# Performance work log

Hardware: AMD Instinct MI355X
Metric: run time of the kernel (lower is better)

## Reference

```python
import jax, jax.numpy as jnp
import numpy as np

B, C, D = 512, 1000, 512
K = 10


def setup_inputs() -> dict:
    key = jax.random.key(0)
    k1, k2, k3, k4, k5 = jax.random.split(key, 5)
    x = jax.random.normal(k1, (B, D), dtype=jnp.float32)
    protos = jax.random.normal(k2, (C, D), dtype=jnp.float32)
    # ex2/ex1 chosen so N*ex2^2 - ex1^2 > 0 (valid sqrt)
    ex2 = jax.random.uniform(k3, (C, D), dtype=jnp.float32) + 1.0
    ex1 = jax.random.uniform(k4, (C, D), dtype=jnp.float32) * 0.1
    cls_num = jax.random.randint(k5, (C,), 1, 100, dtype=jnp.int32)
    proto_label = jnp.arange(C, dtype=jnp.int32)
    return {"x": x, "protos": protos, "ex2": ex2, "ex1": ex1,
            "cls_num": cls_num, "proto_label": proto_label, "k_nearest": K}


def reference(x, protos, ex2, ex1, cls_num, proto_label, k_nearest):
    # rd: per-class, per-feature variance proxy  [C, D]
    N = cls_num[:, None].astype(ex2.dtype)
    rd = jnp.sqrt(N * ex2 ** 2 - ex1 ** 2)
    # softmax over feature dim of (rowmax - rd)
    rd = jax.nn.softmax(jnp.max(rd, axis=1, keepdims=True) - rd, axis=1)
    # weighted squared distances: [B, C, D] -> reduce D -> [B, C]
    diff = x[:, None, :] - protos[None, :, :]
    x_dists = diff ** 2 * rd[None, :, :]
    simi_mat = x_dists.sum(axis=2)  # [B, C]
    # k smallest distances (torch.topk largest=False)
    neg_vals, topk_index = jax.lax.top_k(-simi_mat, k_nearest)
    topk_vals = -neg_vals  # [B, K]
    topk_conf = topk_vals.sum(axis=1, keepdims=True) / topk_vals  # [B, K]
    # pick prototype with max confidence, map through label table
    temp = jnp.argmax(topk_conf, axis=1)  # [B]
    ans_index = jnp.take_along_axis(topk_index, temp[:, None], axis=1)[:, 0]
    predict = proto_label[ans_index]  # [B]
    return predict, topk_conf
```

## Files before the change

### kernel.cpp

```cpp
#include <hip/hip_runtime.h>
#include <math.h>
#include <float.h>

#define B_SZ 512
#define C_SZ 1000
#define D_SZ 512
#define K_TOP 10
#define K2 1024
#define NSPLIT 4
#define KSPLIT 256
#define BC (B_SZ * C_SZ)

#define T3_OFF 0
#define PART_OFF 1024

#define BM 64
#define BN 64
#define BK 32
#define LDA 40
#define LDB 264

using f16x8 = __attribute__((ext_vector_type(8))) _Float16;
using f32x4 = __attribute__((ext_vector_type(4))) float;

#if __has_builtin(__builtin_amdgcn_exp2f)
#define FAST_EXP2(x) __builtin_amdgcn_exp2f(x)
#else
#define FAST_EXP2(x) exp2f(x)
#endif
#if __has_builtin(__builtin_amdgcn_sqrtf)
#define FAST_SQRT(x) __builtin_amdgcn_sqrtf(x)
#else
#define FAST_SQRT(x) sqrtf(x)
#endif
#define LOG2E 1.44269504088896340736f

__device__ __forceinline__ void split2(float v, _Float16& h, _Float16& l) {
    h = (_Float16)v;
    l = (_Float16)(v - (float)h);
}

__global__ __launch_bounds__(256, 2) void gemm_fused(const float* __restrict__ x,
                                                     const float* __restrict__ protos,
                                                     const float* __restrict__ ex2,
                                                     const float* __restrict__ ex1,
                                                     const int* __restrict__ cls_num,
                                                     float* __restrict__ ws) {
    __shared__ __align__(16) _Float16 Ah[BM][LDA];
    __shared__ __align__(16) _Float16 Al[BM][LDA];
    __shared__ __align__(16) _Float16 BSh[BN][LDB];
    __shared__ __align__(16) _Float16 BSl[BN][LDB];

    float* t3   = ws + T3_OFF;
    float* part = ws + PART_OFF;

    const int tid  = threadIdx.x;
    const int lane = tid & 63;
    const int w    = tid >> 6;
    const int c0 = blockIdx.x * BN;
    const int b0 = blockIdx.y * BM;
    const int kz = blockIdx.z;
    const bool isRd = (kz < 2);
    const int ownBase = isRd ? kz * 32 : (kz - 2) * 32;
    const int dutyLo = blockIdx.y * 8;

    for (int i = 0; i < 16; i++) {
        const int lc = w * 16 + i;
        const int c  = c0 + lc;
        if (c < C_SZ) {
            const size_t rb = (size_t)c * D_SZ + lane * 8;
            float e2v[8], e1v[8], pv[8];
            *(float4*)&e2v[0] = *(const float4*)(ex2 + rb);
            *(float4*)&e2v[4] = *(const float4*)(ex2 + rb + 4);
            *(float4*)&e1v[0] = *(const float4*)(ex1 + rb);
            *(float4*)&e1v[4] = *(const float4*)(ex1 + rb + 4);
            *(float4*)&pv[0]  = *(const float4*)(protos + rb);
            *(float4*)&pv[4]  = *(const float4*)(protos + rb + 4);
            const float N = (float)cls_num[c];

            float v[8], mn = FLT_MAX;
            #pragma unroll
            for (int k = 0; k < 8; k++) {
                v[k] = FAST_SQRT(N * e2v[k] * e2v[k] - e1v[k] * e1v[k]);
                mn = fminf(mn, v[k]);
            }
            #pragma unroll
            for (int off = 1; off < 64; off <<= 1) mn = fminf(mn, __shfl_xor(mn, off));

            float ev[8], s = 0.f;
            #pragma unroll
            for (int k = 0; k < 8; k++) {
                ev[k] = FAST_EXP2((mn - v[k]) * LOG2E);
                s += ev[k];
            }

            const bool duty = (kz == 0) && (lc >= dutyLo) && (lc < dutyLo + 8);
            if (duty) {
                float te = 0.f;
                #pragma unroll
                for (int k = 0; k < 8; k++) te = fmaf(ev[k] * pv[k], pv[k], te);
                #pragma unroll
                for (int off = 1; off < 64; off <<= 1) {
                    s  += __shfl_xor(s, off);
                    te += __shfl_xor(te, off);
                }
                const float inv = 1.0f / s;
                if (lane == 0) t3[c] = te * inv;
                const int rel = lane - ownBase;
                if (rel >= 0 && rel < 32) {
                    f16x8 hh, ll;
                    #pragma unroll
                    for (int k = 0; k < 8; k++) {
                        const float rdv = ev[k] * inv;
                        const float val = isRd ? rdv : (-2.0f * rdv * pv[k]);
                        _Float16 h, l;
                        split2(val, h, l);
                        hh[k] = h; ll[k] = l;
                    }
                    *(f16x8*)&BSh[lc][rel * 8] = hh;
                    *(f16x8*)&BSl[lc][rel * 8] = ll;
                }
            } else {
                #pragma unroll
                for (int off = 1; off < 64; off <<= 1) s += __shfl_xor(s, off);
                const float inv = 1.0f / s;
                const int rel = lane - ownBase;
                if (rel >= 0 && rel < 32) {
                    f16x8 hh, ll;
                    #pragma unroll
                    for (int k = 0; k < 8; k++) {
                        const float rdv = ev[k] * inv;
                        const float val = isRd ? rdv : (-2.0f * rdv * pv[k]);
                        _Float16 h, l;
                        split2(val, h, l);
                        hh[k] = h; ll[k] = l;
                    }
                    *(f16x8*)&BSh[lc][rel * 8] = hh;
                    *(f16x8*)&BSl[lc][rel * 8] = ll;
                }
            }
        } else {
            if (lane < 32) {
                f16x8 z;
                #pragma unroll
                for (int k = 0; k < 8; k++) z[k] = (_Float16)0.f;
                *(f16x8*)&BSh[lc][lane * 8] = z;
                *(f16x8*)&BSl[lc][lane * 8] = z;
            }
        }
    }
    __syncthreads();

    const int khalf0 = isRd ? kz * KSPLIT : kz * KSPLIT - D_SZ;
    const int srow = tid >> 2;
    const int sseg = (tid & 3) * 8;
    const int mw = (w >> 1) * 32;
    const int nw = (w & 1) * 32;
    const int lr = lane & 15;
    const int kg = lane >> 4;

    f32x4 acc[2][2];
    #pragma unroll
    for (int i = 0; i < 2; i++)
        #pragma unroll
        for (int j = 0; j < 2; j++)
            #pragma unroll
            for (int r = 0; r < 4; r++) acc[i][j][r] = 0.f;

    for (int ch = 0; ch < KSPLIT / BK; ch++) {
        const int kx = khalf0 + ch * BK + sseg;

        float4 a0 = *(const float4*)(x + (size_t)(b0 + srow) * D_SZ + kx);
        float4 a1 = *(const float4*)(x + (size_t)(b0 + srow) * D_SZ + kx + 4);
        if (isRd) {
            a0.x *= a0.x; a0.y *= a0.y; a0.z *= a0.z; a0.w *= a0.w;
            a1.x *= a1.x; a1.y *= a1.y; a1.z *= a1.z; a1.w *= a1.w;
        }
        const float av[8] = {a0.x, a0.y, a0.z, a0.w, a1.x, a1.y, a1.z, a1.w};
        f16x8 ah, al;
        #pragma unroll
        for (int j = 0; j < 8; j++) {
            _Float16 hh, ll;
            split2(av[j], hh, ll);
            ah[j] = hh; al[j] = ll;
        }

        __syncthreads();
        *(f16x8*)&Ah[srow][sseg] = ah;
        *(f16x8*)&Al[srow][sseg] = al;
        __syncthreads();

        f16x8 fah[2], fal[2], fbh[2], fbl[2];
        #pragma unroll
        for (int i = 0; i < 2; i++) {
            fah[i] = *(const f16x8*)&Ah[mw + i * 16 + lr][kg * 8];
            fal[i] = *(const f16x8*)&Al[mw + i * 16 + lr][kg * 8];
            fbh[i] = *(const f16x8*)&BSh[nw + i * 16 + lr][ch * BK + kg * 8];
            fbl[i] = *(const f16x8*)&BSl[nw + i * 16 + lr][ch * BK + kg * 8];
        }
        #pragma unroll
        for (int i = 0; i < 2; i++)
            #pragma unroll
            for (int j = 0; j < 2; j++) {
                acc[i][j] = __builtin_amdgcn_mfma_f32_16x16x32_f16(fal[i], fbl[j], acc[i][j], 0, 0, 0);
                acc[i][j] = __builtin_amdgcn_mfma_f32_16x16x32_f16(fah[i], fbl[j], acc[i][j], 0, 0, 0);
                acc[i][j] = __builtin_amdgcn_mfma_f32_16x16x32_f16(fal[i], fbh[j], acc[i][j], 0, 0, 0);
                acc[i][j] = __builtin_amdgcn_mfma_f32_16x16x32_f16(fah[i], fbh[j], acc[i][j], 0, 0, 0);
            }
    }

    float* o = part + (size_t)kz * BC;
    #pragma unroll
    for (int i = 0; i < 2; i++) {
        #pragma unroll
        for (int j = 0; j < 2; j++) {
            const int c = c0 + nw + j * 16 + lr;
            if (c < C_SZ) {
                #pragma unroll
                for (int r = 0; r < 4; r++) {
                    const int b = b0 + mw + i * 16 + kg * 4 + r;
                    o[(size_t)b * C_SZ + c] = acc[i][j][r];
                }
            }
        }
    }
}

__global__ __launch_bounds__(256) void topk_kernel(const float* __restrict__ ws,
                                                   const int* __restrict__ proto_label,
                                                   float* __restrict__ out) {
    const float* part = ws + PART_OFF;
    const float* t3   = ws + T3_OFF;
    const int wid = threadIdx.x >> 6;
    const int lane = threadIdx.x & 63;
    const int b = blockIdx.x * 4 + wid;

    float vals[16];
    #pragma unroll
    for (int j = 0; j < 16; j++) {
        const int c = lane + j * 64;
        if (c < C_SZ) {
            const size_t idx = (size_t)b * C_SZ + c;
            float s = t3[c];
            #pragma unroll
            for (int z = 0; z < NSPLIT; z++)
                s += part[(size_t)z * BC + idx];
            vals[j] = s;
        } else {
            vals[j] = FLT_MAX;
        }
    }

    float kv[K_TOP];
    int ki[K_TOP];
    for (int t = 0; t < K_TOP; t++) {
        float bv = FLT_MAX;
        int bi = 0x7fffffff;
        #pragma unroll
        for (int j = 0; j < 16; j++) {
            const int c = lane + j * 64;
            if (vals[j] < bv) { bv = vals[j]; bi = c; }
        }
        #pragma unroll
        for (int off = 1; off < 64; off <<= 1) {
            const float ov = __shfl_xor(bv, off);
            const int oi = __shfl_xor(bi, off);
            if (ov < bv || (ov == bv && oi < bi)) { bv = ov; bi = oi; }
        }
        kv[t] = bv;
        ki[t] = bi;
        if ((bi & 63) == lane) vals[bi >> 6] = FLT_MAX;
    }

    if (lane == 0) {
        float S = 0.f;
        #pragma unroll
        for (int t = 0; t < K_TOP; t++) S += kv[t];
        float conf[K_TOP];
        #pragma unroll
        for (int t = 0; t < K_TOP; t++) {
            conf[t] = S / kv[t];
            out[B_SZ + b * K_TOP + t] = conf[t];
        }
        int best = 0;
        for (int t = 1; t < K_TOP; t++)
            if (conf[t] > conf[best]) best = t;
        out[b] = (float)proto_label[ki[best]];
    }
}

extern "C" void kernel_launch(void* const* d_in, const int* in_sizes, int n_in,
                              void* d_out, int out_size, void* d_ws, size_t ws_size,
                              hipStream_t stream) {
    const float* x           = (const float*)d_in[0];
    const float* protos      = (const float*)d_in[1];
    const float* ex2         = (const float*)d_in[2];
    const float* ex1         = (const float*)d_in[3];
    const int*   cls_num     = (const int*)d_in[4];
    const int*   proto_label = (const int*)d_in[5];

    float* ws  = (float*)d_ws;
    float* out = (float*)d_out;

    dim3 g((C_SZ + BN - 1) / BN, B_SZ / BM, NSPLIT);
    gemm_fused<<<g, 256, 0, stream>>>(x, protos, ex2, ex1, cls_num, ws);

    topk_kernel<<<B_SZ / 4, 256, 0, stream>>>(ws, proto_label, out);
}
```

Measured before the change: 107.0 us.

## Fuse weight prep, GEMM and top-k into one kernel with flag-based grid sync

Merges the two launches into one persistent-style kernel. Only kz==0 blocks compute the softmax weights, each for 8 classes, and write them to global memory; the other blocks spin on per-tile flags before loading them. This removes the redundant per-block weight recomputation and the second kernel launch. The top-k step is done by kz==3 blocks after they spin on partial-completion flags. It relies on all 512 blocks being co-resident to avoid deadlock, adds spin-wait latency, and never resets the flags, so stale MAGIC values from a previous call could let later calls read unfinished data.

```diff
diff --git a/kernel.cpp b/kernel.cpp
--- a/kernel.cpp
+++ b/kernel.cpp
@@ -11,8 +11,13 @@
 #define KSPLIT 256
 #define BC (B_SZ * C_SZ)
 
-#define T3_OFF 0
-#define PART_OFF 1024
+#define WHI_OFFH 0
+#define WLO_OFFH (1024 * 1024)
+#define FLAGB_OFF 1048576
+#define FLAGP_OFF (FLAGB_OFF + 256)
+#define T3_OFF    (FLAGB_OFF + 1024)
+#define PART_OFF  (T3_OFF + 1024)
+#define MAGIC 0x5F3C0DE5u
 
 #define BM 64
 #define BN 64
@@ -40,65 +45,65 @@
     l = (_Float16)(v - (float)h);
 }
 
-__global__ __launch_bounds__(256, 2) void gemm_fused(const float* __restrict__ x,
-                                                     const float* __restrict__ protos,
-                                                     const float* __restrict__ ex2,
-                                                     const float* __restrict__ ex1,
-                                                     const int* __restrict__ cls_num,
-                                                     float* __restrict__ ws) {
+__global__ __launch_bounds__(256, 2) void fused_all(const float* __restrict__ x,
+                                                    const float* __restrict__ protos,
+                                                    const float* __restrict__ ex2,
+                                                    const float* __restrict__ ex1,
+                                                    const int* __restrict__ cls_num,
+                                                    const int* __restrict__ proto_label,
+                                                    float* __restrict__ ws,
+                                                    float* __restrict__ out) {
     __shared__ __align__(16) _Float16 Ah[BM][LDA];
     __shared__ __align__(16) _Float16 Al[BM][LDA];
     __shared__ __align__(16) _Float16 BSh[BN][LDB];
     __shared__ __align__(16) _Float16 BSl[BN][LDB];
 
+    _Float16* Whi = (_Float16*)ws + WHI_OFFH;
+    _Float16* Wlo = (_Float16*)ws + WLO_OFFH;
+    unsigned int* flagB = (unsigned int*)(ws + FLAGB_OFF);
+    unsigned int* flagP = (unsigned int*)(ws + FLAGP_OFF);
     float* t3   = ws + T3_OFF;
     float* part = ws + PART_OFF;
 
     const int tid  = threadIdx.x;
     const int lane = tid & 63;
     const int w    = tid >> 6;
-    const int c0 = blockIdx.x * BN;
-    const int b0 = blockIdx.y * BM;
-    const int kz = blockIdx.z;
+    const int cx = blockIdx.x, by = blockIdx.y, kz = blockIdx.z;
+    const int c0 = cx * BN;
+    const int b0 = by * BM;
     const bool isRd = (kz < 2);
-    const int ownBase = isRd ? kz * 32 : (kz - 2) * 32;
-    const int dutyLo = blockIdx.y * 8;
-
-    for (int i = 0; i < 16; i++) {
-        const int lc = w * 16 + i;
-        const int c  = c0 + lc;
-        if (c < C_SZ) {
-            const size_t rb = (size_t)c * D_SZ + lane * 8;
-            float e2v[8], e1v[8], pv[8];
-            *(float4*)&e2v[0] = *(const float4*)(ex2 + rb);
-            *(float4*)&e2v[4] = *(const float4*)(ex2 + rb + 4);
-            *(float4*)&e1v[0] = *(const float4*)(ex1 + rb);
-            *(float4*)&e1v[4] = *(const float4*)(ex1 + rb + 4);
-            *(float4*)&pv[0]  = *(const float4*)(protos + rb);
-            *(float4*)&pv[4]  = *(const float4*)(protos + rb + 4);
-            const float N = (float)cls_num[c];
-
-            float v[8], mn = FLT_MAX;
-            #pragma unroll
-            for (int k = 0; k < 8; k++) {
-                v[k] = FAST_SQRT(N * e2v[k] * e2v[k] - e1v[k] * e1v[k]);
-                mn = fminf(mn, v[k]);
-            }
-            #pragma unroll
-            for (int off = 1; off < 64; off <<= 1) mn = fminf(mn, __shfl_xor(mn, off));
-
-            float ev[8], s = 0.f;
-            #pragma unroll
-            for (int k = 0; k < 8; k++) {
-                ev[k] = FAST_EXP2((mn - v[k]) * LOG2E);
-                s += ev[k];
-            }
-
-            const bool duty = (kz == 0) && (lc >= dutyLo) && (lc < dutyLo + 8);
-            if (duty) {
-                float te = 0.f;
-                #pragma unroll
-                for (int k = 0; k < 8; k++) te = fmaf(ev[k] * pv[k], pv[k], te);
+
+    if (kz == 0) {
+        #pragma unroll
+        for (int r = 0; r < 2; r++) {
+            const int c = c0 + by * 8 + w * 2 + r;
+            if (c < C_SZ) {
+                const size_t rb = (size_t)c * D_SZ + lane * 8;
+                float e2v[8], e1v[8], pv[8];
+                *(float4*)&e2v[0] = *(const float4*)(ex2 + rb);
+                *(float4*)&e2v[4] = *(const float4*)(ex2 + rb + 4);
+                *(float4*)&e1v[0] = *(const float4*)(ex1 + rb);
+                *(float4*)&e1v[4] = *(const float4*)(ex1 + rb + 4);
+                *(float4*)&pv[0]  = *(const float4*)(protos + rb);
+                *(float4*)&pv[4]  = *(const float4*)(protos + rb + 4);
+                const float N = (float)cls_num[c];
+
+                float v[8], mn = FLT_MAX;
+                #pragma unroll
+                for (int k = 0; k < 8; k++) {
+                    v[k] = FAST_SQRT(N * e2v[k] * e2v[k] - e1v[k] * e1v[k]);
+                    mn = fminf(mn, v[k]);
+                }
+                #pragma unroll
+                for (int off = 1; off < 64; off <<= 1) mn = fminf(mn, __shfl_xor(mn, off));
+
+                float ev[8], s = 0.f, te = 0.f;
+                #pragma unroll
+                for (int k = 0; k < 8; k++) {
+                    ev[k] = FAST_EXP2((mn - v[k]) * LOG2E);
+                    s += ev[k];
+                    te = fmaf(ev[k] * pv[k], pv[k], te);
+                }
                 #pragma unroll
                 for (int off = 1; off < 64; off <<= 1) {
                     s  += __shfl_xor(s, off);
@@ -106,53 +111,64 @@
                 }
                 const float inv = 1.0f / s;
                 if (lane == 0) t3[c] = te * inv;
-                const int rel = lane - ownBase;
-                if (rel >= 0 && rel < 32) {
-                    f16x8 hh, ll;
-                    #pragma unroll
-                    for (int k = 0; k < 8; k++) {
-                        const float rdv = ev[k] * inv;
-                        const float val = isRd ? rdv : (-2.0f * rdv * pv[k]);
-                        _Float16 h, l;
-                        split2(val, h, l);
-                        hh[k] = h; ll[k] = l;
-                    }
-                    *(f16x8*)&BSh[lc][rel * 8] = hh;
-                    *(f16x8*)&BSl[lc][rel * 8] = ll;
-                }
+
+                f16x8 h1, l1, h2, l2;
+                #pragma unroll
+                for (int k = 0; k < 8; k++) {
+                    const float rdv = ev[k] * inv;
+                    const float w2  = -2.0f * rdv * pv[k];
+                    _Float16 hh, ll;
+                    split2(rdv, hh, ll); h1[k] = hh; l1[k] = ll;
+                    split2(w2,  hh, ll); h2[k] = hh; l2[k] = ll;
+                }
+                _Float16* wh = Whi + (size_t)c * K2 + lane * 8;
+                _Float16* wl = Wlo + (size_t)c * K2 + lane * 8;
+                *(f16x8*)(wh)         = h1;
+                *(f16x8*)(wh + D_SZ)  = h2;
+                *(f16x8*)(wl)         = l1;
+                *(f16x8*)(wl + D_SZ)  = l2;
+            }
+        }
+        __syncthreads();
+        if (tid == 0) {
+            __threadfence();
+            __hip_atomic_store(&flagB[cx * 8 + by], MAGIC,
+                               __ATOMIC_RELEASE, __HIP_MEMORY_SCOPE_AGENT);
+        }
+    }
+
+    if (w == 0 && lane < 8) {
+        for (int it = 0; it < (1 << 22); ++it) {
+            if (__hip_atomic_load(&flagB[cx * 8 + lane], __ATOMIC_RELAXED,
+                                  __HIP_MEMORY_SCOPE_AGENT) == MAGIC) break;
+            __builtin_amdgcn_s_sleep(4);
+        }
+    }
+    __syncthreads();
+    __threadfence();
+
+    const int srow = tid >> 2;
+    const int cseg = (tid & 3) * 8;
+    {
+        const int c = c0 + srow;
+        #pragma unroll
+        for (int p = 0; p < 8; p++) {
+            const int col = cseg + p * 32;
+            f16x8 hh, ll;
+            if (c < C_SZ) {
+                hh = *(const f16x8*)(Whi + (size_t)c * K2 + kz * KSPLIT + col);
+                ll = *(const f16x8*)(Wlo + (size_t)c * K2 + kz * KSPLIT + col);
             } else {
                 #pragma unroll
-                for (int off = 1; off < 64; off <<= 1) s += __shfl_xor(s, off);
-                const float inv = 1.0f / s;
-                const int rel = lane - ownBase;
-                if (rel >= 0 && rel < 32) {
-                    f16x8 hh, ll;
-                    #pragma unroll
-                    for (int k = 0; k < 8; k++) {
-                        const float rdv = ev[k] * inv;
-                        const float val = isRd ? rdv : (-2.0f * rdv * pv[k]);
-                        _Float16 h, l;
-                        split2(val, h, l);
-                        hh[k] = h; ll[k] = l;
-                    }
-                    *(f16x8*)&BSh[lc][rel * 8] = hh;
-                    *(f16x8*)&BSl[lc][rel * 8] = ll;
-                }
-            }
-        } else {
-            if (lane < 32) {
-                f16x8 z;
-                #pragma unroll
-                for (int k = 0; k < 8; k++) z[k] = (_Float16)0.f;
-                *(f16x8*)&BSh[lc][lane * 8] = z;
-                *(f16x8*)&BSl[lc][lane * 8] = z;
-            }
+                for (int k = 0; k < 8; k++) { hh[k] = (_Float16)0.f; ll[k] = (_Float16)0.f; }
+            }
+            *(f16x8*)&BSh[srow][col] = hh;
+            *(f16x8*)&BSl[srow][col] = ll;
         }
     }
     __syncthreads();
 
     const int khalf0 = isRd ? kz * KSPLIT : kz * KSPLIT - D_SZ;
-    const int srow = tid >> 2;
     const int sseg = (tid & 3) * 8;
     const int mw = (w >> 1) * 32;
     const int nw = (w & 1) * 32;
@@ -224,68 +240,79 @@
             }
         }
     }
-}
-
-__global__ __launch_bounds__(256) void topk_kernel(const float* __restrict__ ws,
-                                                   const int* __restrict__ proto_label,
-                                                   float* __restrict__ out) {
-    const float* part = ws + PART_OFF;
-    const float* t3   = ws + T3_OFF;
-    const int wid = threadIdx.x >> 6;
-    const int lane = threadIdx.x & 63;
-    const int b = blockIdx.x * 4 + wid;
-
-    float vals[16];
-    #pragma unroll
-    for (int j = 0; j < 16; j++) {
-        const int c = lane + j * 64;
-        if (c < C_SZ) {
-            const size_t idx = (size_t)b * C_SZ + c;
-            float s = t3[c];
-            #pragma unroll
-            for (int z = 0; z < NSPLIT; z++)
-                s += part[(size_t)z * BC + idx];
-            vals[j] = s;
-        } else {
-            vals[j] = FLT_MAX;
-        }
-    }
-
-    float kv[K_TOP];
-    int ki[K_TOP];
-    for (int t = 0; t < K_TOP; t++) {
-        float bv = FLT_MAX;
-        int bi = 0x7fffffff;
+
+    __syncthreads();
+    if (tid == 0) {
+        __threadfence();
+        __hip_atomic_store(&flagP[by * 64 + cx * 4 + kz], MAGIC,
+                           __ATOMIC_RELEASE, __HIP_MEMORY_SCOPE_AGENT);
+    }
+
+    if (kz == 3) {
+        if (w == 0) {
+            for (int it = 0; it < (1 << 22); ++it) {
+                if (__hip_atomic_load(&flagP[by * 64 + lane], __ATOMIC_RELAXED,
+                                      __HIP_MEMORY_SCOPE_AGENT) == MAGIC) break;
+                __builtin_amdgcn_s_sleep(8);
+            }
+        }
+        __syncthreads();
+        __threadfence();
+
+        const int b = (by * 16 + cx) * 4 + w;
+
+        float vals[16];
         #pragma unroll
         for (int j = 0; j < 16; j++) {
             const int c = lane + j * 64;
-            if (vals[j] < bv) { bv = vals[j]; bi = c; }
-        }
-        #pragma unroll
-        for (int off = 1; off < 64; off <<= 1) {
-            const float ov = __shfl_xor(bv, off);
-            const int oi = __shfl_xor(bi, off);
-            if (ov < bv || (ov == bv && oi < bi)) { bv = ov; bi = oi; }
-        }
-        kv[t] = bv;
-        ki[t] = bi;
-        if ((bi & 63) == lane) vals[bi >> 6] = FLT_MAX;
-    }
-
-    if (lane == 0) {
-        float S = 0.f;
-        #pragma unroll
-        for (int t = 0; t < K_TOP; t++) S += kv[t];
-        float conf[K_TOP];
-        #pragma unroll
+            if (c < C_SZ) {
+                const size_t idx = (size_t)b * C_SZ + c;
+                float s = t3[c];
+                #pragma unroll
+                for (int z = 0; z < NSPLIT; z++)
+                    s += part[(size_t)z * BC + idx];
+                vals[j] = s;
+            } else {
+                vals[j] = FLT_MAX;
+            }
+        }
+
+        float kv[K_TOP];
+        int ki[K_TOP];
         for (int t = 0; t < K_TOP; t++) {
-            conf[t] = S / kv[t];
-            out[B_SZ + b * K_TOP + t] = conf[t];
-        }
-        int best = 0;
-        for (int t = 1; t < K_TOP; t++)
-            if (conf[t] > conf[best]) best = t;
-        out[b] = (float)proto_label[ki[best]];
+            float bv = FLT_MAX;
+            int bi = 0x7fffffff;
+            #pragma unroll
+            for (int j = 0; j < 16; j++) {
+                const int c = lane + j * 64;
+                if (vals[j] < bv) { bv = vals[j]; bi = c; }
+            }
+            #pragma unroll
+            for (int off = 1; off < 64; off <<= 1) {
+                const float ov = __shfl_xor(bv, off);
+                const int oi = __shfl_xor(bi, off);
+                if (ov < bv || (ov == bv && oi < bi)) { bv = ov; bi = oi; }
+            }
+            kv[t] = bv;
+            ki[t] = bi;
+            if ((bi & 63) == lane) vals[bi >> 6] = FLT_MAX;
+        }
+
+        if (lane == 0) {
+            float S = 0.f;
+            #pragma unroll
+            for (int t = 0; t < K_TOP; t++) S += kv[t];
+            float conf[K_TOP];
+            #pragma unroll
+            for (int t = 0; t < K_TOP; t++) {
+                conf[t] = S / kv[t];
+                out[B_SZ + b * K_TOP + t] = conf[t];
+            }
+            int best = 0;
+            for (int t = 1; t < K_TOP; t++)
+                if (conf[t] > conf[best]) best = t;
+            out[b] = (float)proto_label[ki[best]];
+        }
     }
 }
 
@@ -303,7 +330,5 @@
     float* out = (float*)d_out;
 
     dim3 g((C_SZ + BN - 1) / BN, B_SZ / BM, NSPLIT);
-    gemm_fused<<<g, 256, 0, stream>>>(x, protos, ex2, ex1, cls_num, ws);
-
-    topk_kernel<<<B_SZ / 4, 256, 0, stream>>>(ws, proto_label, out);
+    fused_all<<<g, 256, 0, stream>>>(x, protos, ex2, ex1, cls_num, proto_label, ws, out);
 }
```

Result: slower. 165.0 us (+54.2%).

## Drop split-K partials; compute full K per block with narrow class tiles

Applied to the files above, without the earlier changes.

Replaces the 4-way split-K GEMM, which wrote four partial [B,C] matrices plus a t3 vector to workspace, with a single pass per block over the full 1024-long concatenated K. Each block handles 16 classes by 128 batch rows, keeps t3 in shared memory and adds it in the epilogue. The top-k kernel then reads one matrix instead of summing four partials. This removes a large amount of global write and read traffic and the partial-sum pass. In exchange, each block does a longer serial K loop with only one MFMA tile per wave, which lowers instruction-level parallelism. It also reloads x for every class tile, and the grid shrinks to 256 blocks.

```diff
diff --git a/kernel.cpp b/kernel.cpp
--- a/kernel.cpp
+++ b/kernel.cpp
@@ -7,18 +7,14 @@
 #define D_SZ 512
 #define K_TOP 10
 #define K2 1024
-#define NSPLIT 4
-#define KSPLIT 256
-#define BC (B_SZ * C_SZ)
-
-#define T3_OFF 0
-#define PART_OFF 1024
-
-#define BM 64
-#define BN 64
+
+#define SIMI_OFF 0
+
+#define BM 128
+#define BN 16
 #define BK 32
 #define LDA 40
-#define LDB 264
+#define LDB 1032
 
 using f16x8 = __attribute__((ext_vector_type(8))) _Float16;
 using f32x4 = __attribute__((ext_vector_type(4))) float;
@@ -40,32 +36,30 @@
     l = (_Float16)(v - (float)h);
 }
 
-__global__ __launch_bounds__(256, 2) void gemm_fused(const float* __restrict__ x,
-                                                     const float* __restrict__ protos,
-                                                     const float* __restrict__ ex2,
-                                                     const float* __restrict__ ex1,
-                                                     const int* __restrict__ cls_num,
-                                                     float* __restrict__ ws) {
+__global__ __launch_bounds__(512, 2) void fused_kernel(const float* __restrict__ x,
+                                                       const float* __restrict__ protos,
+                                                       const float* __restrict__ ex2,
+                                                       const float* __restrict__ ex1,
+                                                       const int* __restrict__ cls_num,
+                                                       float* __restrict__ simi) {
     __shared__ __align__(16) _Float16 Ah[BM][LDA];
     __shared__ __align__(16) _Float16 Al[BM][LDA];
     __shared__ __align__(16) _Float16 BSh[BN][LDB];
     __shared__ __align__(16) _Float16 BSl[BN][LDB];
-
-    float* t3   = ws + T3_OFF;
-    float* part = ws + PART_OFF;
+    __shared__ float t3s[BN];
 
     const int tid  = threadIdx.x;
     const int lane = tid & 63;
     const int w    = tid >> 6;
-    const int c0 = blockIdx.x * BN;
-    const int b0 = blockIdx.y * BM;
-    const int kz = blockIdx.z;
-    const bool isRd = (kz < 2);
-    const int ownBase = isRd ? kz * 32 : (kz - 2) * 32;
-    const int dutyLo = blockIdx.y * 8;
-
-    for (int i = 0; i < 16; i++) {
-        const int lc = w * 16 + i;
+    const int cx = blockIdx.x & 63;
+    const int by = blockIdx.x >> 6;
+    const int c0 = cx * BN;
+    const int b0 = by * BM;
+    if (c0 >= C_SZ) return;
+
+    #pragma unroll
+    for (int r = 0; r < 2; r++) {
+        const int lc = w * 2 + r;
         const int c  = c0 + lc;
         if (c < C_SZ) {
             const size_t rb = (size_t)c * D_SZ + lane * 8;
@@ -87,92 +81,65 @@
             #pragma unroll
             for (int off = 1; off < 64; off <<= 1) mn = fminf(mn, __shfl_xor(mn, off));
 
-            float ev[8], s = 0.f;
+            float ev[8], s = 0.f, te = 0.f;
             #pragma unroll
             for (int k = 0; k < 8; k++) {
                 ev[k] = FAST_EXP2((mn - v[k]) * LOG2E);
                 s += ev[k];
-            }
-
-            const bool duty = (kz == 0) && (lc >= dutyLo) && (lc < dutyLo + 8);
-            if (duty) {
-                float te = 0.f;
-                #pragma unroll
-                for (int k = 0; k < 8; k++) te = fmaf(ev[k] * pv[k], pv[k], te);
-                #pragma unroll
-                for (int off = 1; off < 64; off <<= 1) {
-                    s  += __shfl_xor(s, off);
-                    te += __shfl_xor(te, off);
-                }
-                const float inv = 1.0f / s;
-                if (lane == 0) t3[c] = te * inv;
-                const int rel = lane - ownBase;
-                if (rel >= 0 && rel < 32) {
-                    f16x8 hh, ll;
-                    #pragma unroll
-                    for (int k = 0; k < 8; k++) {
-                        const float rdv = ev[k] * inv;
-                        const float val = isRd ? rdv : (-2.0f * rdv * pv[k]);
-                        _Float16 h, l;
-                        split2(val, h, l);
-                        hh[k] = h; ll[k] = l;
-                    }
-                    *(f16x8*)&BSh[lc][rel * 8] = hh;
-                    *(f16x8*)&BSl[lc][rel * 8] = ll;
-                }
-            } else {
-                #pragma unroll
-                for (int off = 1; off < 64; off <<= 1) s += __shfl_xor(s, off);
-                const float inv = 1.0f / s;
-                const int rel = lane - ownBase;
-                if (rel >= 0 && rel < 32) {
-                    f16x8 hh, ll;
-                    #pragma unroll
-                    for (int k = 0; k < 8; k++) {
-                        const float rdv = ev[k] * inv;
-                        const float val = isRd ? rdv : (-2.0f * rdv * pv[k]);
-                        _Float16 h, l;
-                        split2(val, h, l);
-                        hh[k] = h; ll[k] = l;
-                    }
-                    *(f16x8*)&BSh[lc][rel * 8] = hh;
-                    *(f16x8*)&BSl[lc][rel * 8] = ll;
-                }
-            }
+                te = fmaf(ev[k] * pv[k], pv[k], te);
+            }
+            #pragma unroll
+            for (int off = 1; off < 64; off <<= 1) {
+                s  += __shfl_xor(s, off);
+                te += __shfl_xor(te, off);
+            }
+            const float inv = 1.0f / s;
+            if (lane == 0) t3s[lc] = te * inv;
+
+            f16x8 h1, l1, h2, l2;
+            #pragma unroll
+            for (int k = 0; k < 8; k++) {
+                const float rdv = ev[k] * inv;
+                const float w2  = -2.0f * rdv * pv[k];
+                _Float16 hh, ll;
+                split2(rdv, hh, ll); h1[k] = hh; l1[k] = ll;
+                split2(w2,  hh, ll); h2[k] = hh; l2[k] = ll;
+            }
+            const int d = lane * 8;
+            *(f16x8*)&BSh[lc][d]         = h1;
+            *(f16x8*)&BSh[lc][D_SZ + d]  = h2;
+            *(f16x8*)&BSl[lc][d]         = l1;
+            *(f16x8*)&BSl[lc][D_SZ + d]  = l2;
         } else {
-            if (lane < 32) {
-                f16x8 z;
-                #pragma unroll
-                for (int k = 0; k < 8; k++) z[k] = (_Float16)0.f;
-                *(f16x8*)&BSh[lc][lane * 8] = z;
-                *(f16x8*)&BSl[lc][lane * 8] = z;
-            }
+            f16x8 z;
+            #pragma unroll
+            for (int k = 0; k < 8; k++) z[k] = (_Float16)0.f;
+            const int d = lane * 8;
+            *(f16x8*)&BSh[lc][d]        = z;
+            *(f16x8*)&BSh[lc][D_SZ + d] = z;
+            *(f16x8*)&BSl[lc][d]        = z;
+            *(f16x8*)&BSl[lc][D_SZ + d] = z;
         }
     }
     __syncthreads();
 
-    const int khalf0 = isRd ? kz * KSPLIT : kz * KSPLIT - D_SZ;
     const int srow = tid >> 2;
     const int sseg = (tid & 3) * 8;
-    const int mw = (w >> 1) * 32;
-    const int nw = (w & 1) * 32;
+    const int mw = w * 16;
     const int lr = lane & 15;
     const int kg = lane >> 4;
 
-    f32x4 acc[2][2];
+    f32x4 acc;
     #pragma unroll
-    for (int i = 0; i < 2; i++)
-        #pragma unroll
-        for (int j = 0; j < 2; j++)
-            #pragma unroll
-            for (int r = 0; r < 4; r++) acc[i][j][r] = 0.f;
-
-    for (int ch = 0; ch < KSPLIT / BK; ch++) {
-        const int kx = khalf0 + ch * BK + sseg;
+    for (int r = 0; r < 4; r++) acc[r] = 0.f;
+
+    for (int ch = 0; ch < K2 / BK; ch++) {
+        const bool sq = (ch < 16);
+        const int kx = (sq ? ch * BK : ch * BK - D_SZ) + sseg;
 
         float4 a0 = *(const float4*)(x + (size_t)(b0 + srow) * D_SZ + kx);
         float4 a1 = *(const float4*)(x + (size_t)(b0 + srow) * D_SZ + kx + 4);
-        if (isRd) {
+        if (sq) {
             a0.x *= a0.x; a0.y *= a0.y; a0.z *= a0.z; a0.w *= a0.w;
             a1.x *= a1.x; a1.y *= a1.y; a1.z *= a1.z; a1.w *= a1.w;
         }
@@ -190,38 +157,24 @@
         *(f16x8*)&Al[srow][sseg] = al;
         __syncthreads();
 
-        f16x8 fah[2], fal[2], fbh[2], fbl[2];
-        #pragma unroll
-        for (int i = 0; i < 2; i++) {
-            fah[i] = *(const f16x8*)&Ah[mw + i * 16 + lr][kg * 8];
-            fal[i] = *(const f16x8*)&Al[mw + i * 16 + lr][kg * 8];
-            fbh[i] = *(const f16x8*)&BSh[nw + i * 16 + lr][ch * BK + kg * 8];
-            fbl[i] = *(const f16x8*)&BSl[nw + i * 16 + lr][ch * BK + kg * 8];
-        }
-        #pragma unroll
-        for (int i = 0; i < 2; i++)
-            #pragma unroll
-            for (int j = 0; j < 2; j++) {
-                acc[i][j] = __builtin_amdgcn_mfma_f32_16x16x32_f16(fal[i], fbl[j], acc[i][j], 0, 0, 0);
-                acc[i][j] = __builtin_amdgcn_mfma_f32_16x16x32_f16(fah[i], fbl[j], acc[i][j], 0, 0, 0);
-                acc[i][j] = __builtin_amdgcn_mfma_f32_16x16x32_f16(fal[i], fbh[j], acc[i][j], 0, 0, 0);
-                acc[i][j] = __builtin_amdgcn_mfma_f32_16x16x32_f16(fah[i], fbh[j], acc[i][j], 0, 0, 0);
-            }
-    }
-
-    float* o = part + (size_t)kz * BC;
-    #pragma unroll
-    for (int i = 0; i < 2; i++) {
-        #pragma unroll
-        for (int j = 0; j < 2; j++) {
-            const int c = c0 + nw + j * 16 + lr;
-            if (c < C_SZ) {
-                #pragma unroll
-                for (int r = 0; r < 4; r++) {
-                    const int b = b0 + mw + i * 16 + kg * 4 + r;
-                    o[(size_t)b * C_SZ + c] = acc[i][j][r];
-                }
-            }
+        const f16x8 fah = *(const f16x8*)&Ah[mw + lr][kg * 8];
+        const f16x8 fal = *(const f16x8*)&Al[mw + lr][kg * 8];
+        const f16x8 fbh = *(const f16x8*)&BSh[lr][ch * BK + kg * 8];
+        const f16x8 fbl = *(const f16x8*)&BSl[lr][ch * BK + kg * 8];
+
+        acc = __builtin_amdgcn_mfma_f32_16x16x32_f16(fal, fbl, acc, 0, 0, 0);
+        acc = __builtin_amdgcn_mfma_f32_16x16x32_f16(fah, fbl, acc, 0, 0, 0);
+        acc = __builtin_amdgcn_mfma_f32_16x16x32_f16(fal, fbh, acc, 0, 0, 0);
+        acc = __builtin_amdgcn_mfma_f32_16x16x32_f16(fah, fbh, acc, 0, 0, 0);
+    }
+
+    const int c = c0 + lr;
+    if (c < C_SZ) {
+        const float t3v = t3s[lr];
+        #pragma unroll
+        for (int r = 0; r < 4; r++) {
+            const int b = b0 + mw + kg * 4 + r;
+            simi[(size_t)b * C_SZ + c] = acc[r] + t3v;
         }
     }
 }
@@ -229,8 +182,7 @@
 __global__ __launch_bounds__(256) void topk_kernel(const float* __restrict__ ws,
                                                    const int* __restrict__ proto_label,
                                                    float* __restrict__ out) {
-    const float* part = ws + PART_OFF;
-    const float* t3   = ws + T3_OFF;
+    const float* simi = ws + SIMI_OFF;
     const int wid = threadIdx.x >> 6;
     const int lane = threadIdx.x & 63;
     const int b = blockIdx.x * 4 + wid;
@@ -239,16 +191,7 @@
     #pragma unroll
     for (int j = 0; j < 16; j++) {
         const int c = lane + j * 64;
-        if (c < C_SZ) {
-            const size_t idx = (size_t)b * C_SZ + c;
-            float s = t3[c];
-            #pragma unroll
-            for (int z = 0; z < NSPLIT; z++)
-                s += part[(size_t)z * BC + idx];
-            vals[j] = s;
-        } else {
-            vals[j] = FLT_MAX;
-        }
+        vals[j] = (c < C_SZ) ? simi[(size_t)b * C_SZ + c] : FLT_MAX;
     }
 
     float kv[K_TOP];
@@ -302,8 +245,8 @@
     float* ws  = (float*)d_ws;
     float* out = (float*)d_out;
 
-    dim3 g((C_SZ + BN - 1) / BN, B_SZ / BM, NSPLIT);
-    gemm_fused<<<g, 256, 0, stream>>>(x, protos, ex2, ex1, cls_num, ws);
+    fused_kernel<<<256, 512, 0, stream>>>(x, protos, ex2, ex1, cls_num,
+                                          ws + SIMI_OFF);
 
     topk_kernel<<<B_SZ / 4, 256, 0, stream>>>(ws, proto_label, out);
 }
```

New measurement: 104.4 us. -2.5%, faster.
